# Optimization experiments

Measured on AMD Instinct MI355X. Metric: run time of the kernel, lower is better.

## Reference

```python
import jax, jax.numpy as jnp
import numpy as np

T, D = 8192, 1024      # num flattened tokens, hidden_dim
E, K = 8, 2            # n_experts, num_experts_per_tok


def setup_inputs() -> dict:
    key = jax.random.key(0)
    k1, k2, k3, k4, k5 = jax.random.split(key, 5)
    x = jax.random.normal(k1, (T, D), dtype=jnp.float32)
    flat_expert_indices = jax.random.randint(k2, (T * K,), 0, E, dtype=jnp.int32)
    flat_expert_weights = jax.random.uniform(k3, (T * K,), dtype=jnp.float32)
    # Expert params: fc1/fc2 are bias-free Linears, stored torch-style [out, in]
    W1 = jax.random.normal(k4, (E, D, D), dtype=jnp.float32) * (1.0 / np.sqrt(D))
    W2 = jax.random.normal(k5, (E, D, D), dtype=jnp.float32) * (1.0 / np.sqrt(D))
    return {"x": x, "flat_expert_indices": flat_expert_indices,
            "flat_expert_weights": flat_expert_weights, "W1": W1, "W2": W2}


def reference(x, flat_expert_indices, flat_expert_weights, W1, W2):
    # DummyExpert: relu(relu(x @ W1.T) @ W2.T), per expert (torch Linear = x @ W.T)
    # Dense dispatch: compute every expert on every token, then gather the
    # top-k expert outputs per token and combine with routing weights.
    h = jax.nn.relu(jnp.einsum('td,eod->eto', x, W1))   # [E, T, D]
    y = jax.nn.relu(jnp.einsum('eto,epo->etp', h, W2))  # [E, T, D]
    idx = flat_expert_indices.reshape(T, K)             # [T, K]
    w = flat_expert_weights.reshape(T, K)               # [T, K]
    yt = jnp.transpose(y, (1, 0, 2))                    # [T, E, D]
    sel = jnp.take_along_axis(yt, idx[:, :, None].astype(jnp.int32), axis=1)  # [T, K, D]
    return jnp.sum(sel * w[:, :, None], axis=1)         # [T, D]
```

## Files before the change

kernel.cpp:

```cpp
#include <hip/hip_runtime.h>

typedef unsigned short u16;
typedef unsigned int   u32;
typedef unsigned long long u64;
typedef __attribute__((ext_vector_type(8))) short short8;
typedef __attribute__((ext_vector_type(4))) float f32x4;

#define T_TOK 8192
#define DIM   1024
#define NEXP  8
#define NPAIR (T_TOK * 2)
#define MAXTILES 72
#define NCASTBLK 12288

__device__ __forceinline__ u16 f2bf(float f) {
  u32 u = __builtin_bit_cast(u32, f);
  u32 r = (u + 0x7fffu + ((u >> 16) & 1u)) >> 16;
  return (u16)r;
}
__device__ __forceinline__ float bf2f(u16 b) {
  return __builtin_bit_cast(float, ((u32)b) << 16);
}

__device__ __forceinline__ void gl_lds16(const u16* g, u16* l) {
  __builtin_amdgcn_global_load_lds(
      (const __attribute__((address_space(1))) u32*)g,
      (__attribute__((address_space(3))) u32*)l,
      16, 0, 0);
}

__global__ void cast_sort_k(const float* __restrict__ x, const float* __restrict__ W1,
                            const float* __restrict__ W2,
                            u16* __restrict__ xb, u16* __restrict__ w1b, u16* __restrict__ w2b,
                            const int* __restrict__ idx,
                            int* __restrict__ counts, int* __restrict__ offsets,
                            int* __restrict__ bucket, int* __restrict__ pos,
                            int* __restrict__ tlist, int* __restrict__ ntiles) {
  if (blockIdx.x < NCASTBLK) {
    const int g = (blockIdx.x * 256 + threadIdx.x) * 8;
    const int region = g >> 23;
    const int i = g & 0x7fffff;
    const float* s = (region == 0) ? x : (region == 1) ? W1 : W2;
    u16* d = (region == 0) ? xb : (region == 1) ? w1b : w2b;
    f32x4 a = *(const f32x4*)(s + i);
    f32x4 b = *(const f32x4*)(s + i + 4);
    short8 o;
    o[0] = (short)f2bf(a[0]); o[1] = (short)f2bf(a[1]);
    o[2] = (short)f2bf(a[2]); o[3] = (short)f2bf(a[3]);
    o[4] = (short)f2bf(b[0]); o[5] = (short)f2bf(b[1]);
    o[6] = (short)f2bf(b[2]); o[7] = (short)f2bf(b[3]);
    *(short8*)(d + i) = o;
    return;
  }

  __shared__ int lc[4][NEXP];
  __shared__ int lo[4][NEXP];
  const int tid  = threadIdx.x;
  const int w    = tid >> 6;
  const int lane = tid & 63;
  const u64 ltmask = (lane == 63) ? 0x7fffffffffffffffull : ((1ull << lane) - 1);

  int cnt[NEXP] = {};
  for (int i = 0; i < 64; ++i) {
    const int e = idx[w * 4096 + i * 64 + lane];
#pragma unroll
    for (int ex = 0; ex < NEXP; ++ex) {
      u64 m = __ballot(e == ex);
      cnt[ex] += (int)__popcll(m);
    }
  }
  if (lane == 0) {
#pragma unroll
    for (int ex = 0; ex < NEXP; ++ex) lc[w][ex] = cnt[ex];
  }
  __syncthreads();

  if (tid == 0) {
    int s = 0;
    int c8[NEXP];
    for (int ex = 0; ex < NEXP; ++ex) {
      offsets[ex] = s;
      int c = 0;
      for (int ww = 0; ww < 4; ++ww) { lo[ww][ex] = s; s += lc[ww][ex]; c += lc[ww][ex]; }
      counts[ex] = c;
      c8[ex] = c;
    }
    int t = 0;
    for (int r = 0; r < 64; ++r)
      for (int ex = 0; ex < NEXP; ++ex)
        if (r * 256 < c8[ex]) tlist[t++] = (r << 3) | ex;
    *ntiles = t;
  }
  __syncthreads();

  int cur[NEXP];
#pragma unroll
  for (int ex = 0; ex < NEXP; ++ex) cur[ex] = lo[w][ex];
  for (int i = 0; i < 64; ++i) {
    const int item = w * 4096 + i * 64 + lane;
    const int e = idx[item];
    int p = 0;
#pragma unroll
    for (int ex = 0; ex < NEXP; ++ex) {
      u64 m = __ballot(e == ex);
      int rank = (int)__popcll(m & ltmask);
      if (e == ex) p = cur[ex] + rank;
      cur[ex] += (int)__popcll(m);
    }
    bucket[p] = item;
    pos[item] = p;
  }
}

template <int GATHER>
__global__ __launch_bounds__(512, 4)
void moe_gemm_k(const u16* __restrict__ A,
                const u16* __restrict__ W,
                u16* __restrict__ O,
                const int* __restrict__ counts,
                const int* __restrict__ offsets,
                const int* __restrict__ bucket,
                const int* __restrict__ tlist,
                const int* __restrict__ ntiles) {
  if ((int)blockIdx.x >= *ntiles) return;
  const int info = tlist[blockIdx.x];
  const int e    = info & 7;
  const int m0   = (info >> 3) << 8;
  const int cnt  = counts[e];
  const int seg  = offsets[e];
  const int n0   = blockIdx.y << 7;

  __shared__ u16 As[256 * 64];
  __shared__ u16 Bs[128 * 64];

  const int tid  = threadIdx.x;
  const int lane = tid & 63;
  const int wave = tid >> 6;

  int aoff[4], boff[2];
#pragma unroll
  for (int j = 0; j < 4; ++j) {
    const int c   = ((wave << 2) + j) * 64 + lane;
    const int r   = c >> 3;
    const int c16 = (c & 7) ^ (r & 7);
    int p = seg + m0 + r;
    p = (p < seg + cnt) ? p : (seg + cnt - 1);
    int rowbase;
    if (GATHER) { const int pair = bucket[p]; rowbase = (pair >> 1) * DIM; }
    else        { rowbase = p * DIM; }
    aoff[j] = rowbase + (c16 << 3);
  }
#pragma unroll
  for (int j = 0; j < 2; ++j) {
    const int c   = ((wave << 1) + j) * 64 + lane;
    const int r   = c >> 3;
    const int c16 = (c & 7) ^ (r & 7);
    boff[j] = e * DIM * DIM + (n0 + r) * DIM + (c16 << 3);
  }

  f32x4 acc[4][4] = {};

  const int wm   = (wave >> 1) << 6;
  const int wn   = (wave & 1) << 6;
  const int lr   = lane & 15;
  const int quad = lane >> 4;

  for (int k0 = 0; k0 < DIM; k0 += 64) {
    __syncthreads();
#pragma unroll
    for (int j = 0; j < 4; ++j)
      gl_lds16(A + aoff[j] + k0, &As[((wave << 2) + j) << 9]);
#pragma unroll
    for (int j = 0; j < 2; ++j)
      gl_lds16(W + boff[j] + k0, &Bs[((wave << 1) + j) << 9]);
    __syncthreads();

#pragma unroll
    for (int kk = 0; kk < 64; kk += 32) {
      const int qb = (kk >> 3) + quad;
      short8 af[4], bf[4];
#pragma unroll
      for (int mi = 0; mi < 4; ++mi) {
        const int r = wm + (mi << 4) + lr;
        af[mi] = *(const short8*)&As[r * 64 + ((qb ^ (r & 7)) << 3)];
      }
#pragma unroll
      for (int ni = 0; ni < 4; ++ni) {
        const int r = wn + (ni << 4) + lr;
        bf[ni] = *(const short8*)&Bs[r * 64 + ((qb ^ (r & 7)) << 3)];
      }
#pragma unroll
      for (int mi = 0; mi < 4; ++mi)
#pragma unroll
        for (int ni = 0; ni < 4; ++ni)
          acc[mi][ni] = __builtin_amdgcn_mfma_f32_16x16x32_bf16(af[mi], bf[ni], acc[mi][ni], 0, 0, 0);
    }
  }

  const int pend = seg + cnt;
#pragma unroll
  for (int mi = 0; mi < 4; ++mi) {
#pragma unroll
    for (int ni = 0; ni < 4; ++ni) {
      const int col = n0 + wn + (ni << 4) + lr;
#pragma unroll
      for (int r4 = 0; r4 < 4; ++r4) {
        const int p = seg + m0 + wm + (mi << 4) + (quad << 2) + r4;
        if (p < pend) {
          float v = acc[mi][ni][r4];
          v = v > 0.f ? v : 0.f;
          O[(size_t)p * DIM + col] = f2bf(v);
        }
      }
    }
  }
}

__global__ void combine_k(const u16* __restrict__ y, const int* __restrict__ pos,
                          const float* __restrict__ wts, float* __restrict__ out) {
  const int t    = blockIdx.x * 2 + (threadIdx.x >> 7);
  const int lane = threadIdx.x & 127;
  const int col  = lane * 8;
  const int p0 = pos[2 * t], p1 = pos[2 * t + 1];
  const float w0 = wts[2 * t], w1 = wts[2 * t + 1];
  const short8 a = *(const short8*)(y + (size_t)p0 * DIM + col);
  const short8 b = *(const short8*)(y + (size_t)p1 * DIM + col);
  f32x4 o0, o1;
#pragma unroll
  for (int j = 0; j < 8; ++j) {
    float v = w0 * bf2f((u16)a[j]) + w1 * bf2f((u16)b[j]);
    if (j < 4) o0[j] = v; else o1[j - 4] = v;
  }
  float* op = out + (size_t)t * DIM + col;
  *(f32x4*)op = o0;
  *(f32x4*)(op + 4) = o1;
}

extern "C" void kernel_launch(void* const* d_in, const int* in_sizes, int n_in,
                              void* d_out, int out_size, void* d_ws, size_t ws_size,
                              hipStream_t stream) {
  const float* x   = (const float*)d_in[0];
  const int*   idx = (const int*)d_in[1];
  const float* wts = (const float*)d_in[2];
  const float* W1  = (const float*)d_in[3];
  const float* W2  = (const float*)d_in[4];
  float* out = (float*)d_out;

  char* ws = (char*)d_ws;
  int* counts  = (int*)ws;
  int* offsets = (int*)(ws + 32);
  int* ntiles  = (int*)(ws + 64);
  int* tlist   = (int*)(ws + 128);
  int* bucket  = (int*)(ws + 1024);
  int* pos     = (int*)(ws + 1024 + 4 * NPAIR);
  const size_t base = 132096;
  const size_t MB16 = 16ull * 1024 * 1024;
  u16* xb  = (u16*)(ws + base);
  u16* w1b = (u16*)(ws + base + MB16);
  u16* w2b = (u16*)(ws + base + 2 * MB16);
  u16* h   = (u16*)(ws + base + 3 * MB16);
  u16* yb  = xb;

  cast_sort_k<<<NCASTBLK + 1, 256, 0, stream>>>(x, W1, W2, xb, w1b, w2b,
                                                idx, counts, offsets, bucket, pos,
                                                tlist, ntiles);

  dim3 gg(MAXTILES, DIM / 128);
  moe_gemm_k<1><<<gg, 512, 0, stream>>>(xb, w1b, h, counts, offsets, bucket, tlist, ntiles);
  moe_gemm_k<0><<<gg, 512, 0, stream>>>(h, w2b, yb, counts, offsets, bucket, tlist, ntiles);

  combine_k<<<T_TOK / 2, 256, 0, stream>>>(yb, pos, wts, out);
}
```

Measured before the change: 302.2 us.

## Fuse weighted combine into second GEMM epilogue via atomic scatter-add

Removes the separate combine kernel. The second expert GEMM now atomically adds weighted ReLU outputs straight into the fp32 output, which the prep kernel zero-fills. The bf16 intermediate y write/read and the pos array go away. The prep kernel moves to 1024-thread blocks and loads the routing indices into registers once instead of twice. In exchange, the epilogue issues many scattered fp32 atomics, which may contend and makes the summation order nondeterministic.

```diff
diff --git a/kernel.cpp b/kernel.cpp
--- a/kernel.cpp
+++ b/kernel.cpp
@@ -11,15 +11,13 @@
 #define NEXP  8
 #define NPAIR (T_TOK * 2)
 #define MAXTILES 72
-#define NCASTBLK 12288
+#define CASTBLK 3072
+#define ZEROBLK 1024
 
 __device__ __forceinline__ u16 f2bf(float f) {
   u32 u = __builtin_bit_cast(u32, f);
   u32 r = (u + 0x7fffu + ((u >> 16) & 1u)) >> 16;
   return (u16)r;
-}
-__device__ __forceinline__ float bf2f(u16 b) {
-  return __builtin_bit_cast(float, ((u32)b) << 16);
 }
 
 __device__ __forceinline__ void gl_lds16(const u16* g, u16* l) {
@@ -29,15 +27,18 @@
       16, 0, 0);
 }
 
-__global__ void cast_sort_k(const float* __restrict__ x, const float* __restrict__ W1,
-                            const float* __restrict__ W2,
-                            u16* __restrict__ xb, u16* __restrict__ w1b, u16* __restrict__ w2b,
-                            const int* __restrict__ idx,
-                            int* __restrict__ counts, int* __restrict__ offsets,
-                            int* __restrict__ bucket, int* __restrict__ pos,
-                            int* __restrict__ tlist, int* __restrict__ ntiles) {
-  if (blockIdx.x < NCASTBLK) {
-    const int g = (blockIdx.x * 256 + threadIdx.x) * 8;
+__global__ __launch_bounds__(1024)
+void prep_k(const float* __restrict__ x, const float* __restrict__ W1,
+            const float* __restrict__ W2,
+            u16* __restrict__ xb, u16* __restrict__ w1b, u16* __restrict__ w2b,
+            const int* __restrict__ idx,
+            int* __restrict__ counts, int* __restrict__ offsets,
+            int* __restrict__ bucket,
+            int* __restrict__ tlist, int* __restrict__ ntiles,
+            float* __restrict__ out) {
+  const int tid = threadIdx.x;
+  if (blockIdx.x >= 1 && blockIdx.x <= CASTBLK) {
+    const int g = ((int)blockIdx.x - 1) * 8192 + tid * 8;
     const int region = g >> 23;
     const int i = g & 0x7fffff;
     const float* s = (region == 0) ? x : (region == 1) ? W1 : W2;
@@ -52,20 +53,30 @@
     *(short8*)(d + i) = o;
     return;
   }
-
-  __shared__ int lc[4][NEXP];
-  __shared__ int lo[4][NEXP];
-  const int tid  = threadIdx.x;
+  if (blockIdx.x > CASTBLK) {
+    const int i = ((int)blockIdx.x - CASTBLK - 1) * 8192 + tid * 8;
+    f32x4 z = {0.f, 0.f, 0.f, 0.f};
+    *(f32x4*)(out + i) = z;
+    *(f32x4*)(out + i + 4) = z;
+    return;
+  }
+
+  __shared__ int lc[16][NEXP];
+  __shared__ int lo[16][NEXP];
   const int w    = tid >> 6;
   const int lane = tid & 63;
   const u64 ltmask = (lane == 63) ? 0x7fffffffffffffffull : ((1ull << lane) - 1);
 
+  int e_i[16];
+#pragma unroll
+  for (int i = 0; i < 16; ++i) e_i[i] = idx[(w * 16 + i) * 64 + lane];
+
   int cnt[NEXP] = {};
-  for (int i = 0; i < 64; ++i) {
-    const int e = idx[w * 4096 + i * 64 + lane];
+#pragma unroll
+  for (int i = 0; i < 16; ++i) {
 #pragma unroll
     for (int ex = 0; ex < NEXP; ++ex) {
-      u64 m = __ballot(e == ex);
+      u64 m = __ballot(e_i[i] == ex);
       cnt[ex] += (int)__popcll(m);
     }
   }
@@ -81,7 +92,7 @@
     for (int ex = 0; ex < NEXP; ++ex) {
       offsets[ex] = s;
       int c = 0;
-      for (int ww = 0; ww < 4; ++ww) { lo[ww][ex] = s; s += lc[ww][ex]; c += lc[ww][ex]; }
+      for (int ww = 0; ww < 16; ++ww) { lo[ww][ex] = s; s += lc[ww][ex]; c += lc[ww][ex]; }
       counts[ex] = c;
       c8[ex] = c;
     }
@@ -96,9 +107,10 @@
   int cur[NEXP];
 #pragma unroll
   for (int ex = 0; ex < NEXP; ++ex) cur[ex] = lo[w][ex];
-  for (int i = 0; i < 64; ++i) {
-    const int item = w * 4096 + i * 64 + lane;
-    const int e = idx[item];
+#pragma unroll
+  for (int i = 0; i < 16; ++i) {
+    const int item = (w * 16 + i) * 64 + lane;
+    const int e = e_i[i];
     int p = 0;
 #pragma unroll
     for (int ex = 0; ex < NEXP; ++ex) {
@@ -108,15 +120,16 @@
       cur[ex] += (int)__popcll(m);
     }
     bucket[p] = item;
-    pos[item] = p;
-  }
-}
-
-template <int GATHER>
+  }
+}
+
+template <int GATHER, int SCATTER>
 __global__ __launch_bounds__(512, 4)
 void moe_gemm_k(const u16* __restrict__ A,
                 const u16* __restrict__ W,
                 u16* __restrict__ O,
+                float* __restrict__ out,
+                const float* __restrict__ wts,
                 const int* __restrict__ counts,
                 const int* __restrict__ offsets,
                 const int* __restrict__ bucket,
@@ -201,12 +214,24 @@
 #pragma unroll
   for (int mi = 0; mi < 4; ++mi) {
 #pragma unroll
-    for (int ni = 0; ni < 4; ++ni) {
-      const int col = n0 + wn + (ni << 4) + lr;
-#pragma unroll
-      for (int r4 = 0; r4 < 4; ++r4) {
-        const int p = seg + m0 + wm + (mi << 4) + (quad << 2) + r4;
-        if (p < pend) {
+    for (int r4 = 0; r4 < 4; ++r4) {
+      const int p = seg + m0 + wm + (mi << 4) + (quad << 2) + r4;
+      if (p >= pend) continue;
+      if (SCATTER) {
+        const int pair = bucket[p];
+        const float wv = wts[pair];
+        float* orow = out + (size_t)(pair >> 1) * DIM;
+#pragma unroll
+        for (int ni = 0; ni < 4; ++ni) {
+          const int col = n0 + wn + (ni << 4) + lr;
+          float v = acc[mi][ni][r4];
+          v = v > 0.f ? v : 0.f;
+          atomicAdd(orow + col, wv * v);
+        }
+      } else {
+#pragma unroll
+        for (int ni = 0; ni < 4; ++ni) {
+          const int col = n0 + wn + (ni << 4) + lr;
           float v = acc[mi][ni][r4];
           v = v > 0.f ? v : 0.f;
           O[(size_t)p * DIM + col] = f2bf(v);
@@ -214,26 +239,6 @@
       }
     }
   }
-}
-
-__global__ void combine_k(const u16* __restrict__ y, const int* __restrict__ pos,
-                          const float* __restrict__ wts, float* __restrict__ out) {
-  const int t    = blockIdx.x * 2 + (threadIdx.x >> 7);
-  const int lane = threadIdx.x & 127;
-  const int col  = lane * 8;
-  const int p0 = pos[2 * t], p1 = pos[2 * t + 1];
-  const float w0 = wts[2 * t], w1 = wts[2 * t + 1];
-  const short8 a = *(const short8*)(y + (size_t)p0 * DIM + col);
-  const short8 b = *(const short8*)(y + (size_t)p1 * DIM + col);
-  f32x4 o0, o1;
-#pragma unroll
-  for (int j = 0; j < 8; ++j) {
-    float v = w0 * bf2f((u16)a[j]) + w1 * bf2f((u16)b[j]);
-    if (j < 4) o0[j] = v; else o1[j - 4] = v;
-  }
-  float* op = out + (size_t)t * DIM + col;
-  *(f32x4*)op = o0;
-  *(f32x4*)(op + 4) = o1;
 }
 
 extern "C" void kernel_launch(void* const* d_in, const int* in_sizes, int n_in,
@@ -252,22 +257,19 @@
   int* ntiles  = (int*)(ws + 64);
   int* tlist   = (int*)(ws + 128);
   int* bucket  = (int*)(ws + 1024);
-  int* pos     = (int*)(ws + 1024 + 4 * NPAIR);
   const size_t base = 132096;
   const size_t MB16 = 16ull * 1024 * 1024;
   u16* xb  = (u16*)(ws + base);
   u16* w1b = (u16*)(ws + base + MB16);
   u16* w2b = (u16*)(ws + base + 2 * MB16);
   u16* h   = (u16*)(ws + base + 3 * MB16);
-  u16* yb  = xb;
-
-  cast_sort_k<<<NCASTBLK + 1, 256, 0, stream>>>(x, W1, W2, xb, w1b, w2b,
-                                                idx, counts, offsets, bucket, pos,
-                                                tlist, ntiles);
+
+  prep_k<<<1 + CASTBLK + ZEROBLK, 1024, 0, stream>>>(
+      x, W1, W2, xb, w1b, w2b, idx, counts, offsets, bucket, tlist, ntiles, out);
 
   dim3 gg(MAXTILES, DIM / 128);
-  moe_gemm_k<1><<<gg, 512, 0, stream>>>(xb, w1b, h, counts, offsets, bucket, tlist, ntiles);
-  moe_gemm_k<0><<<gg, 512, 0, stream>>>(h, w2b, yb, counts, offsets, bucket, tlist, ntiles);
-
-  combine_k<<<T_TOK / 2, 256, 0, stream>>>(yb, pos, wts, out);
-}
+  moe_gemm_k<1, 0><<<gg, 512, 0, stream>>>(xb, w1b, h, nullptr, nullptr,
+                                           counts, offsets, bucket, tlist, ntiles);
+  moe_gemm_k<0, 1><<<gg, 512, 0, stream>>>(h, w2b, nullptr, out, wts,
+                                           counts, offsets, bucket, tlist, ntiles);
+}
```

New measurement: 295.1 us. 1.02x faster.
